# Optimization experiments

Hardware: AMD Instinct MI355X
Metric: run time of the kernel (lower is better)

The kernel has to match this reference:

```python
import jax, jax.numpy as jnp
import numpy as np

N = 100000
E = 1600000
IN_DIM = 128
HEADS = 8
OUT_PER_HEAD = 16  # output_dim // heads = 128 // 8
NEG_SLOPE = 0.2    # PyG GATConv default negative_slope


def setup_inputs() -> dict:
    key = jax.random.key(0)
    k_x, k_ei, k_w, k_as, k_ad, k_b = jax.random.split(key, 6)
    x = jax.random.normal(k_x, (N, IN_DIM), dtype=jnp.float32)
    edge_index = jax.random.randint(k_ei, (2, E), 0, N, dtype=jnp.int64)
    # GATConv params (Glorot-ish scale)
    scale = 1.0 / np.sqrt(IN_DIM)
    W = jax.random.normal(k_w, (IN_DIM, HEADS, OUT_PER_HEAD), dtype=jnp.float32) * scale
    a_src = jax.random.normal(k_as, (HEADS, OUT_PER_HEAD), dtype=jnp.float32) * scale
    a_dst = jax.random.normal(k_ad, (HEADS, OUT_PER_HEAD), dtype=jnp.float32) * scale
    bias = jnp.zeros((HEADS * OUT_PER_HEAD,), dtype=jnp.float32)
    return {"x": x, "edge_index": edge_index, "W": W, "a_src": a_src,
            "a_dst": a_dst, "bias": bias}


def reference(x, edge_index, W, a_src, a_dst, bias):
    # Linear projection per head: [N, H, F]
    xp = jnp.einsum('ni,ihf->nhf', x, W)
    # Per-node attention halves: [N, H]
    al_src = jnp.einsum('nhf,hf->nh', xp, a_src)
    al_dst = jnp.einsum('nhf,hf->nh', xp, a_dst)
    src, dst = edge_index[0], edge_index[1]
    # Edge logits with LeakyReLU: [E, H]
    e = al_src[src] + al_dst[dst]
    e = jnp.where(e >= 0, e, NEG_SLOPE * e)
    # Segment softmax over incoming edges of each dst node
    m = jnp.full((N, HEADS), -jnp.inf, dtype=e.dtype).at[dst].max(e)
    ex = jnp.exp(e - m[dst])
    denom = jnp.zeros((N, HEADS), dtype=e.dtype).at[dst].add(ex)
    alpha = ex / jnp.where(denom[dst] == 0, 1.0, denom[dst])  # [E, H]
    # Weighted scatter-aggregate of source messages: [N, H, F]
    out = jnp.zeros((N, HEADS, OUT_PER_HEAD), dtype=xp.dtype)
    out = out.at[dst].add(xp[src] * alpha[:, :, None])
    # Concat heads, bias, ELU (GATLayer applies F.elu)
    out = out.reshape(N, HEADS * OUT_PER_HEAD) + bias
    return jnp.where(out > 0, out, jnp.expm1(out))
```

## Files before the change

kernel.cpp:

```cpp
#include <hip/hip_runtime.h>
#include <hip/hip_fp16.h>
#include <cstdint>

constexpr int IN_DIM = 128;
constexpr int OUT_DIM = 128;
constexpr int HEADS = 8;
constexpr float NEG_SLOPE = 0.2f;

constexpr int BUCKET_CAP = 5120;
constexpr int BIN_TILE   = 4096;

__global__ __launch_bounds__(256) void proj_kernel(
    const float* __restrict__ x, const float* __restrict__ W,
    const float* __restrict__ a_src, const float* __restrict__ a_dst,
    __half* __restrict__ xp, float* __restrict__ als, float* __restrict__ ald,
    int N)
{
  __shared__ float Wl[128 * 64];
  __shared__ float xs[64 * 128];
  const int t  = threadIdx.x;
  const int ch = blockIdx.y;
  const int r0 = blockIdx.x * 64;

  const float* wbase = W + ch * 64;
#pragma unroll
  for (int j = 0; j < 8; ++j) {
    int lidx = (t + j * 256) * 4;
    int k = lidx >> 6;
    int c = lidx & 63;
    *(float4*)&Wl[lidx] = *(const float4*)&wbase[k * 128 + c];
  }
#pragma unroll
  for (int j = 0; j < 8; ++j) {
    int lidx = (t + j * 256) * 4;
    int row  = lidx >> 7;
    int colf = lidx & 127;
    int c4   = colf >> 2;
    int grow = r0 + row;
    float4 v = make_float4(0.f, 0.f, 0.f, 0.f);
    if (grow < N) v = *(const float4*)&x[(size_t)grow * IN_DIM + colf];
    int pc4 = c4 ^ ((row >> 2) & 3);
    *(float4*)&xs[row * 128 + (pc4 << 2)] = v;
  }
  __syncthreads();

  const int cg  = t & 15;
  const int rg  = t >> 4;
  const int swz = rg & 3;

  float acc[4][4];
#pragma unroll
  for (int i = 0; i < 4; ++i)
#pragma unroll
    for (int j = 0; j < 4; ++j) acc[i][j] = 0.f;

#pragma unroll 2
  for (int kk = 0; kk < 32; ++kk) {
    float4 xv[4], wv[4];
#pragma unroll
    for (int i = 0; i < 4; ++i)
      xv[i] = *(const float4*)&xs[(4 * rg + i) * 128 + ((kk ^ swz) << 2)];
#pragma unroll
    for (int j = 0; j < 4; ++j)
      wv[j] = *(const float4*)&Wl[(4 * kk + j) * 64 + 4 * cg];
#pragma unroll
    for (int i = 0; i < 4; ++i) {
      const float* xi = (const float*)&xv[i];
#pragma unroll
      for (int j = 0; j < 4; ++j) {
        const float* wj = (const float*)&wv[j];
        float xk = xi[j];
#pragma unroll
        for (int c = 0; c < 4; ++c)
          acc[i][c] = fmaf(xk, wj[c], acc[i][c]);
      }
    }
  }

  const int cbase = ch * 64 + 4 * cg;
  float asv[4], adv[4];
  *(float4*)asv = *(const float4*)&a_src[cbase];
  *(float4*)adv = *(const float4*)&a_dst[cbase];
#pragma unroll
  for (int r = 0; r < 4; ++r) {
    int grow = r0 + 4 * rg + r;
    float sp = acc[r][0]*asv[0] + acc[r][1]*asv[1] + acc[r][2]*asv[2] + acc[r][3]*asv[3];
    float dp = acc[r][0]*adv[0] + acc[r][1]*adv[1] + acc[r][2]*adv[2] + acc[r][3]*adv[3];
    sp += __shfl_xor(sp, 1); sp += __shfl_xor(sp, 2);
    dp += __shfl_xor(dp, 1); dp += __shfl_xor(dp, 2);
    if (grow < N) {
      union { __half2 h2[2]; float2 f2; } u;
      u.h2[0] = __floats2half2_rn(acc[r][0], acc[r][1]);
      u.h2[1] = __floats2half2_rn(acc[r][2], acc[r][3]);
      *(float2*)&xp[(size_t)grow * OUT_DIM + cbase] = u.f2;
      if ((cg & 3) == 0) {
        int h = cbase >> 4;
        als[grow * HEADS + h] = sp;
        ald[grow * HEADS + h] = dp;
      }
    }
  }
}

__global__ void detect_kernel(const void* __restrict__ ei, int E, int N,
                              int* __restrict__ flag) {
  const long long* e64 = (const long long*)ei;
  int lane = threadIdx.x;
  int step = E > 64 ? E / 64 : 1;
  size_t idx = ((size_t)lane * step) % (size_t)E;
  long long v = e64[idx];
  int bad = (v < 0 || v >= (long long)N) ? 1 : 0;
  unsigned long long m = __ballot(bad);
  if (lane == 0) *flag = (m == 0ull) ? 1 : 0;
}

__device__ __forceinline__ int load_idx(const void* ei, size_t i, int is64) {
  return is64 ? (int)((const long long*)ei)[i] : ((const int*)ei)[i];
}

__global__ __launch_bounds__(256) void bin_kernel(
    const void* __restrict__ ei, const int* __restrict__ flag,
    int* __restrict__ bucket_cnt, unsigned int* __restrict__ buckets,
    int E)
{
  __shared__ int cnt[512];
  const int is64 = *flag;
  const int t = threadIdx.x;
  cnt[t] = 0; cnt[t + 256] = 0;
  __syncthreads();

  unsigned int rec[16];
  short bk[16];
  const int base_e = blockIdx.x * BIN_TILE;
#pragma unroll
  for (int j = 0; j < 16; ++j) {
    int idx = base_e + j * 256 + t;
    bk[j] = -1;
    if (idx < E) {
      int s = load_idx(ei, (size_t)idx, is64);
      int d = load_idx(ei, (size_t)E + idx, is64);
      rec[j] = ((unsigned)(d & 255) << 24) | (unsigned)s;
      bk[j] = (short)(d >> 8);
      atomicAdd(&cnt[d >> 8], 1);
    }
  }
  __syncthreads();

  int c0 = cnt[t];
  cnt[t] = (c0 > 0) ? atomicAdd(&bucket_cnt[t], c0) : 0;
  int c1 = cnt[t + 256];
  cnt[t + 256] = (c1 > 0) ? atomicAdd(&bucket_cnt[t + 256], c1) : 0;
  __syncthreads();

#pragma unroll
  for (int j = 0; j < 16; ++j) {
    if (bk[j] >= 0) {
      int pos = atomicAdd(&cnt[bk[j]], 1);
      if (pos < BUCKET_CAP)
        buckets[(size_t)bk[j] * BUCKET_CAP + pos] = rec[j];
    }
  }
}

__global__ __launch_bounds__(512) void bucket_scan(const int* __restrict__ bucket_cnt,
                                                   int* __restrict__ bucket_base) {
  __shared__ int lds[512];
  int t = threadIdx.x;
  int v = bucket_cnt[t];
  lds[t] = v;
  __syncthreads();
  for (int d = 1; d < 512; d <<= 1) {
    int u = (t >= d) ? lds[t - d] : 0;
    __syncthreads();
    lds[t] += u;
    __syncthreads();
  }
  bucket_base[t] = lds[t] - v;
  if (t == 511) bucket_base[512] = lds[511];
}

__global__ __launch_bounds__(256) void sort_bucket(
    const unsigned int* __restrict__ buckets, const int* __restrict__ bucket_base,
    int* __restrict__ csr, int* __restrict__ row_off, int N, int E)
{
  __shared__ unsigned int recs[BUCKET_CAP];
  __shared__ int cnt[256];
  __shared__ int sc[256];
  const int b = blockIdx.x;
  const int t = threadIdx.x;
  const int base = bucket_base[b];
  int m = bucket_base[b + 1] - base;
  if (m > BUCKET_CAP) m = BUCKET_CAP;

  cnt[t] = 0;
  __syncthreads();
  for (int i = t; i < m; i += 256) {
    unsigned int r = buckets[(size_t)b * BUCKET_CAP + i];
    recs[i] = r;
    atomicAdd(&cnt[r >> 24], 1);
  }
  __syncthreads();

  sc[t] = cnt[t];
  __syncthreads();
  for (int d = 1; d < 256; d <<= 1) {
    int u = (t >= d) ? sc[t - d] : 0;
    __syncthreads();
    sc[t] += u;
    __syncthreads();
  }
  int excl = sc[t] - cnt[t];

  int n = (b << 8) + t;
  if (n < N) row_off[n] = base + excl;
  if (b == 0 && t == 0) row_off[N] = E;

  cnt[t] = base + excl;
  __syncthreads();
  for (int i = t; i < m; i += 256) {
    unsigned int r = recs[i];
    int pos = atomicAdd(&cnt[r >> 24], 1);
    csr[pos] = (int)(r & 0x00FFFFFFu);
  }
}

__global__ __launch_bounds__(256) void aggregate_kernel(
    const __half* __restrict__ xp, const float* __restrict__ als,
    const float* __restrict__ ald, const int* __restrict__ row_off,
    const int* __restrict__ csr, const float* __restrict__ bias,
    float* __restrict__ out, int N)
{
  int node = blockIdx.x * 4 + (threadIdx.x >> 6);
  if (node >= N) return;
  const int lane = threadIdx.x & 63;
  const int h = lane >> 3;
  const float ad = ald[node * HEADS + h];
  int beg = row_off[node], end = row_off[node + 1];
  beg = __builtin_amdgcn_readfirstlane(beg);
  end = __builtin_amdgcn_readfirstlane(end);
  float acc0 = 0.f, acc1 = 0.f, den = 0.f;
  int i = beg;
  for (; i + 1 < end; i += 2) {
    int s0 = csr[i], s1 = csr[i + 1];
    float as0 = als[s0 * HEADS + h];
    float as1 = als[s1 * HEADS + h];
    __half2 xv0 = *(const __half2*)&xp[(size_t)s0 * OUT_DIM + 2 * lane];
    __half2 xv1 = *(const __half2*)&xp[(size_t)s1 * OUT_DIM + 2 * lane];
    float e0 = as0 + ad; e0 = e0 >= 0.f ? e0 : NEG_SLOPE * e0;
    float e1 = as1 + ad; e1 = e1 >= 0.f ? e1 : NEG_SLOPE * e1;
    float w0 = __expf(e0), w1 = __expf(e1);
    den += w0 + w1;
    float2 f0 = __half22float2(xv0), f1 = __half22float2(xv1);
    acc0 = fmaf(w0, f0.x, acc0); acc1 = fmaf(w0, f0.y, acc1);
    acc0 = fmaf(w1, f1.x, acc0); acc1 = fmaf(w1, f1.y, acc1);
  }
  if (i < end) {
    int s0 = csr[i];
    float as0 = als[s0 * HEADS + h];
    __half2 xv0 = *(const __half2*)&xp[(size_t)s0 * OUT_DIM + 2 * lane];
    float e0 = as0 + ad; e0 = e0 >= 0.f ? e0 : NEG_SLOPE * e0;
    float w0 = __expf(e0);
    den += w0;
    float2 f0 = __half22float2(xv0);
    acc0 = fmaf(w0, f0.x, acc0); acc1 = fmaf(w0, f0.y, acc1);
  }
  float inv = den > 0.f ? 1.f / den : 0.f;
  float2 b = *(const float2*)&bias[2 * lane];
  float v0 = fmaf(acc0, inv, b.x);
  float v1 = fmaf(acc1, inv, b.y);
  float2 o;
  o.x = v0 > 0.f ? v0 : expm1f(v0);
  o.y = v1 > 0.f ? v1 : expm1f(v1);
  *(float2*)&out[(size_t)node * OUT_DIM + 2 * lane] = o;
}

extern "C" void kernel_launch(void* const* d_in, const int* in_sizes, int n_in,
                              void* d_out, int out_size, void* d_ws, size_t ws_size,
                              hipStream_t stream) {
  const float* x      = (const float*)d_in[0];
  const void*  ei     = d_in[1];
  const float* W      = (const float*)d_in[2];
  const float* a_src  = (const float*)d_in[3];
  const float* a_dst  = (const float*)d_in[4];
  const float* bias   = (const float*)d_in[5];
  float* out = (float*)d_out;
  const int N = in_sizes[0] / IN_DIM;
  const int E = in_sizes[1] / 2;
  const int NB  = (N + 255) >> 8;
  const int nbt = (E + BIN_TILE - 1) / BIN_TILE;

  char* ws = (char*)d_ws;
  size_t off = 0;
  __half* xp          = (__half*)(ws + off); off += (size_t)N * OUT_DIM * 2;
  off = (off + 15) & ~(size_t)15;
  float* als          = (float*)(ws + off);  off += (size_t)N * HEADS * 4;
  float* ald          = (float*)(ws + off);  off += (size_t)N * HEADS * 4;
  int*   bucket_cnt   = (int*)(ws + off);    off += 512 * 4;
  int*   bucket_base  = (int*)(ws + off);    off += 516 * 4;
  unsigned int* buckets = (unsigned int*)(ws + off); off += (size_t)512 * BUCKET_CAP * 4;
  int*   csr          = (int*)(ws + off);    off += (size_t)E * 4;
  int*   row_off      = (int*)(ws + off);    off += ((size_t)N + 4) * 4;
  int*   flag         = (int*)(ws + off);    off += 16;

  hipMemsetAsync(bucket_cnt, 0, 512 * 4, stream);
  detect_kernel<<<1, 64, 0, stream>>>(ei, E, N, flag);

  dim3 pgrid((N + 63) / 64, 2);
  proj_kernel<<<pgrid, 256, 0, stream>>>(x, W, a_src, a_dst, xp, als, ald, N);

  bin_kernel<<<nbt, 256, 0, stream>>>(ei, flag, bucket_cnt, buckets, E);
  bucket_scan<<<1, 512, 0, stream>>>(bucket_cnt, bucket_base);
  sort_bucket<<<NB, 256, 0, stream>>>(buckets, bucket_base, csr, row_off, N, E);
  aggregate_kernel<<<(N + 3) / 4, 256, 0, stream>>>(xp, als, ald, row_off, csr,
                                                    bias, out, N);
}
```

Baseline: 286.6 us.

## Use MFMA fp16 for projection, split attention logits, cooperative edge weights in aggregate

Rewrites the projection GEMM to convert x and W to fp16 in swizzled shared memory and compute with 16x16x32 MFMA instructions, staging output through LDS for coalesced stores. Attention logit dot-products move into a separate att_kernel that reads the fp16 xp back. The aggregate kernel now computes edge weights for 8 edges per head-group in parallel lanes and broadcasts them via shuffles, cutting redundant exp/als loads. This trades precision on inputs (fp16 x and W) and adds an extra kernel pass plus shuffle overhead.

```diff
diff --git a/kernel.cpp b/kernel.cpp
--- a/kernel.cpp
+++ b/kernel.cpp
@@ -10,95 +10,114 @@
 constexpr int BUCKET_CAP = 5120;
 constexpr int BIN_TILE   = 4096;
 
+typedef _Float16 f16x8 __attribute__((ext_vector_type(8)));
+typedef float    f32x4 __attribute__((ext_vector_type(4)));
+
 __global__ __launch_bounds__(256) void proj_kernel(
     const float* __restrict__ x, const float* __restrict__ W,
-    const float* __restrict__ a_src, const float* __restrict__ a_dst,
-    __half* __restrict__ xp, float* __restrict__ als, float* __restrict__ ald,
-    int N)
-{
-  __shared__ float Wl[128 * 64];
-  __shared__ float xs[64 * 128];
+    __half* __restrict__ xp, int N)
+{
+  __shared__ __half xs[64 * 128];
+  __shared__ __half Wt[128 * 128];
   const int t  = threadIdx.x;
-  const int ch = blockIdx.y;
   const int r0 = blockIdx.x * 64;
 
-  const float* wbase = W + ch * 64;
-#pragma unroll
-  for (int j = 0; j < 8; ++j) {
-    int lidx = (t + j * 256) * 4;
-    int k = lidx >> 6;
-    int c = lidx & 63;
-    *(float4*)&Wl[lidx] = *(const float4*)&wbase[k * 128 + c];
-  }
-#pragma unroll
-  for (int j = 0; j < 8; ++j) {
-    int lidx = (t + j * 256) * 4;
-    int row  = lidx >> 7;
-    int colf = lidx & 127;
-    int c4   = colf >> 2;
+#pragma unroll
+  for (int it = 0; it < 4; ++it) {
+    int m   = t + it * 256;
+    int row = m >> 4;
+    int g   = m & 15;
     int grow = r0 + row;
-    float4 v = make_float4(0.f, 0.f, 0.f, 0.f);
-    if (grow < N) v = *(const float4*)&x[(size_t)grow * IN_DIM + colf];
-    int pc4 = c4 ^ ((row >> 2) & 3);
-    *(float4*)&xs[row * 128 + (pc4 << 2)] = v;
-  }
-  __syncthreads();
-
-  const int cg  = t & 15;
-  const int rg  = t >> 4;
-  const int swz = rg & 3;
-
-  float acc[4][4];
-#pragma unroll
-  for (int i = 0; i < 4; ++i)
-#pragma unroll
-    for (int j = 0; j < 4; ++j) acc[i][j] = 0.f;
-
-#pragma unroll 2
-  for (int kk = 0; kk < 32; ++kk) {
-    float4 xv[4], wv[4];
-#pragma unroll
-    for (int i = 0; i < 4; ++i)
-      xv[i] = *(const float4*)&xs[(4 * rg + i) * 128 + ((kk ^ swz) << 2)];
-#pragma unroll
-    for (int j = 0; j < 4; ++j)
-      wv[j] = *(const float4*)&Wl[(4 * kk + j) * 64 + 4 * cg];
-#pragma unroll
-    for (int i = 0; i < 4; ++i) {
-      const float* xi = (const float*)&xv[i];
-#pragma unroll
-      for (int j = 0; j < 4; ++j) {
-        const float* wj = (const float*)&wv[j];
-        float xk = xi[j];
-#pragma unroll
-        for (int c = 0; c < 4; ++c)
-          acc[i][c] = fmaf(xk, wj[c], acc[i][c]);
-      }
-    }
-  }
-
-  const int cbase = ch * 64 + 4 * cg;
-  float asv[4], adv[4];
-  *(float4*)asv = *(const float4*)&a_src[cbase];
-  *(float4*)adv = *(const float4*)&a_dst[cbase];
-#pragma unroll
-  for (int r = 0; r < 4; ++r) {
-    int grow = r0 + 4 * rg + r;
-    float sp = acc[r][0]*asv[0] + acc[r][1]*asv[1] + acc[r][2]*asv[2] + acc[r][3]*asv[3];
-    float dp = acc[r][0]*adv[0] + acc[r][1]*adv[1] + acc[r][2]*adv[2] + acc[r][3]*adv[3];
-    sp += __shfl_xor(sp, 1); sp += __shfl_xor(sp, 2);
-    dp += __shfl_xor(dp, 1); dp += __shfl_xor(dp, 2);
+    float4 v0 = make_float4(0.f,0.f,0.f,0.f), v1 = v0;
     if (grow < N) {
-      union { __half2 h2[2]; float2 f2; } u;
-      u.h2[0] = __floats2half2_rn(acc[r][0], acc[r][1]);
-      u.h2[1] = __floats2half2_rn(acc[r][2], acc[r][3]);
-      *(float2*)&xp[(size_t)grow * OUT_DIM + cbase] = u.f2;
-      if ((cg & 3) == 0) {
-        int h = cbase >> 4;
-        als[grow * HEADS + h] = sp;
-        ald[grow * HEADS + h] = dp;
-      }
-    }
+      const float* src = &x[(size_t)grow * IN_DIM + g * 8];
+      v0 = *(const float4*)src;
+      v1 = *(const float4*)(src + 4);
+    }
+    union { __half2 h2[4]; uint4 u; } u;
+    u.h2[0] = __floats2half2_rn(v0.x, v0.y);
+    u.h2[1] = __floats2half2_rn(v0.z, v0.w);
+    u.h2[2] = __floats2half2_rn(v1.x, v1.y);
+    u.h2[3] = __floats2half2_rn(v1.z, v1.w);
+    *(uint4*)&xs[row * 128 + ((g ^ (row & 15)) << 3)] = u.u;
+  }
+#pragma unroll
+  for (int it = 0; it < 16; ++it) {
+    int m  = t + it * 256;
+    int c  = m & 127;
+    int kq = m >> 7;
+    int k  = kq * 4;
+    float w0 = W[(size_t)(k + 0) * OUT_DIM + c];
+    float w1 = W[(size_t)(k + 1) * OUT_DIM + c];
+    float w2 = W[(size_t)(k + 2) * OUT_DIM + c];
+    float w3 = W[(size_t)(k + 3) * OUT_DIM + c];
+    union { __half2 h2[2]; uint2 u; } u;
+    u.h2[0] = __floats2half2_rn(w0, w1);
+    u.h2[1] = __floats2half2_rn(w2, w3);
+    int g = k >> 3;
+    *(uint2*)&Wt[c * 128 + (((g ^ (c & 15)) << 3) + (k & 7))] = u.u;
+  }
+  __syncthreads();
+
+  const int wv = t >> 6;
+  const int l  = t & 63;
+  const int fr = l & 15;
+  const int fq = l >> 4;
+
+  f32x4 acc[8];
+#pragma unroll
+  for (int ct = 0; ct < 8; ++ct) acc[ct] = (f32x4){0.f,0.f,0.f,0.f};
+
+#pragma unroll
+  for (int ks = 0; ks < 4; ++ks) {
+    int g = 4 * ks + fq;
+    f16x8 a = *(const f16x8*)&xs[(16 * wv + fr) * 128 + ((g ^ fr) << 3)];
+#pragma unroll
+    for (int ct = 0; ct < 8; ++ct) {
+      f16x8 b = *(const f16x8*)&Wt[(16 * ct + fr) * 128 + ((g ^ fr) << 3)];
+      acc[ct] = __builtin_amdgcn_mfma_f32_16x16x32_f16(a, b, acc[ct], 0, 0, 0);
+    }
+  }
+  __syncthreads();
+
+#pragma unroll
+  for (int ct = 0; ct < 8; ++ct)
+#pragma unroll
+    for (int r = 0; r < 4; ++r)
+      xs[(16 * wv + 4 * fq + r) * 128 + 16 * ct + fr] = __float2half(acc[ct][r]);
+  __syncthreads();
+
+#pragma unroll
+  for (int it = 0; it < 4; ++it) {
+    int m   = t + it * 256;
+    int row = m >> 4;
+    int u4  = m & 15;
+    int grow = r0 + row;
+    if (grow < N) {
+      uint4 v = *(const uint4*)&xs[row * 128 + u4 * 8];
+      *(uint4*)&xp[(size_t)grow * OUT_DIM + u4 * 8] = v;
+    }
+  }
+}
+
+__global__ __launch_bounds__(256) void att_kernel(
+    const __half* __restrict__ xp, const float* __restrict__ a_src,
+    const float* __restrict__ a_dst, float* __restrict__ als,
+    float* __restrict__ ald, int N)
+{
+  int node = blockIdx.x * 4 + (threadIdx.x >> 6);
+  if (node >= N) return;
+  const int l = threadIdx.x & 63;
+  float2 f  = __half22float2(*(const __half2*)&xp[(size_t)node * OUT_DIM + 2 * l]);
+  float2 as = *(const float2*)&a_src[2 * l];
+  float2 ad = *(const float2*)&a_dst[2 * l];
+  float sp = f.x * as.x + f.y * as.y;
+  float dp = f.x * ad.x + f.y * ad.y;
+  sp += __shfl_xor(sp, 1); sp += __shfl_xor(sp, 2); sp += __shfl_xor(sp, 4);
+  dp += __shfl_xor(dp, 1); dp += __shfl_xor(dp, 2); dp += __shfl_xor(dp, 4);
+  if ((l & 7) == 0) {
+    als[node * HEADS + (l >> 3)] = sp;
+    ald[node * HEADS + (l >> 3)] = dp;
   }
 }
 
@@ -233,38 +252,53 @@
   int node = blockIdx.x * 4 + (threadIdx.x >> 6);
   if (node >= N) return;
   const int lane = threadIdx.x & 63;
+  const int j = lane & 7;
   const int h = lane >> 3;
   const float ad = ald[node * HEADS + h];
   int beg = row_off[node], end = row_off[node + 1];
   beg = __builtin_amdgcn_readfirstlane(beg);
   end = __builtin_amdgcn_readfirstlane(end);
-  float acc0 = 0.f, acc1 = 0.f, den = 0.f;
+
+  float acc0 = 0.f, acc1 = 0.f, den_p = 0.f;
+  const int nfull = (end - beg) & ~7;
+  const int full_end = beg + nfull;
   int i = beg;
-  for (; i + 1 < end; i += 2) {
-    int s0 = csr[i], s1 = csr[i + 1];
-    float as0 = als[s0 * HEADS + h];
-    float as1 = als[s1 * HEADS + h];
-    __half2 xv0 = *(const __half2*)&xp[(size_t)s0 * OUT_DIM + 2 * lane];
-    __half2 xv1 = *(const __half2*)&xp[(size_t)s1 * OUT_DIM + 2 * lane];
-    float e0 = as0 + ad; e0 = e0 >= 0.f ? e0 : NEG_SLOPE * e0;
-    float e1 = as1 + ad; e1 = e1 >= 0.f ? e1 : NEG_SLOPE * e1;
-    float w0 = __expf(e0), w1 = __expf(e1);
-    den += w0 + w1;
-    float2 f0 = __half22float2(xv0), f1 = __half22float2(xv1);
-    acc0 = fmaf(w0, f0.x, acc0); acc1 = fmaf(w0, f0.y, acc1);
-    acc0 = fmaf(w1, f1.x, acc0); acc1 = fmaf(w1, f1.y, acc1);
+  for (; i < full_end; i += 8) {
+    int s = csr[i + j];
+    float as = als[s * HEADS + h];
+    float e = as + ad; e = e >= 0.f ? e : NEG_SLOPE * e;
+    float w = __expf(e);
+    den_p += w;
+#pragma unroll
+    for (int q = 0; q < 8; ++q) {
+      int   sq = __shfl(s, q);
+      float wq = __shfl(w, (lane & 56) | q);
+      float2 f = __half22float2(*(const __half2*)&xp[(size_t)sq * OUT_DIM + 2 * lane]);
+      acc0 = fmaf(wq, f.x, acc0);
+      acc1 = fmaf(wq, f.y, acc1);
+    }
   }
   if (i < end) {
-    int s0 = csr[i];
-    float as0 = als[s0 * HEADS + h];
-    __half2 xv0 = *(const __half2*)&xp[(size_t)s0 * OUT_DIM + 2 * lane];
-    float e0 = as0 + ad; e0 = e0 >= 0.f ? e0 : NEG_SLOPE * e0;
-    float w0 = __expf(e0);
-    den += w0;
-    float2 f0 = __half22float2(xv0);
-    acc0 = fmaf(w0, f0.x, acc0); acc1 = fmaf(w0, f0.y, acc1);
-  }
-  float inv = den > 0.f ? 1.f / den : 0.f;
+    int rem = end - i;
+    int idx = i + j;
+    int s = csr[idx < end ? idx : i];
+    float as = als[s * HEADS + h];
+    float e = as + ad; e = e >= 0.f ? e : NEG_SLOPE * e;
+    float w = (j < rem) ? __expf(e) : 0.f;
+    den_p += w;
+    for (int q = 0; q < rem; ++q) {
+      int   sq = __shfl(s, q);
+      float wq = __shfl(w, (lane & 56) | q);
+      float2 f = __half22float2(*(const __half2*)&xp[(size_t)sq * OUT_DIM + 2 * lane]);
+      acc0 = fmaf(wq, f.x, acc0);
+      acc1 = fmaf(wq, f.y, acc1);
+    }
+  }
+  den_p += __shfl_xor(den_p, 1);
+  den_p += __shfl_xor(den_p, 2);
+  den_p += __shfl_xor(den_p, 4);
+
+  float inv = den_p > 0.f ? 1.f / den_p : 0.f;
   float2 b = *(const float2*)&bias[2 * lane];
   float v0 = fmaf(acc0, inv, b.x);
   float v1 = fmaf(acc1, inv, b.y);
@@ -305,8 +339,8 @@
   hipMemsetAsync(bucket_cnt, 0, 512 * 4, stream);
   detect_kernel<<<1, 64, 0, stream>>>(ei, E, N, flag);
 
-  dim3 pgrid((N + 63) / 64, 2);
-  proj_kernel<<<pgrid, 256, 0, stream>>>(x, W, a_src, a_dst, xp, als, ald, N);
+  proj_kernel<<<(N + 63) / 64, 256, 0, stream>>>(x, W, xp, N);
+  att_kernel<<<(N + 3) / 4, 256, 0, stream>>>(xp, a_src, a_dst, als, ald, N);
 
   bin_kernel<<<nbt, 256, 0, stream>>>(ei, flag, bucket_cnt, buckets, E);
   bucket_scan<<<1, 512, 0, stream>>>(bucket_cnt, bucket_base);
```

New measurement: 256.9 us. -10.3%, faster.
